# Kernel tuning notes

Measured on AMD Instinct MI355X. Metric: run time of the kernel, lower is better.

## Reference

```python
import jax, jax.numpy as jnp
import numpy as np

N_PULSES = 8_000_000
NUM_DOMS = 200_000
EPS = 1e-08


def setup_inputs() -> dict:
    key = jax.random.key(0)
    k1, k2, k3 = jax.random.split(key, 3)
    times = jax.random.normal(k1, (N_PULSES,), dtype=jnp.float32) * 100.0
    charges = jax.random.uniform(k2, (N_PULSES,), dtype=jnp.float32) * 10.0
    dom_idx = jax.random.randint(k3, (N_PULSES,), 0, NUM_DOMS, dtype=jnp.int32)
    return {"times": times, "charges": charges, "dom_idx": dom_idx, "num_doms": NUM_DOMS}


def reference(times, charges, dom_idx, num_doms):
    n = times.shape[0]
    ones = jnp.ones_like(times)
    # per-DOM pulse counts (float, matching torch's float scatter_add of ones)
    count = jnp.zeros((num_doms,), dtype=times.dtype).at[dom_idx].add(ones)

    # --- temporal features ---
    first_times = jnp.full((num_doms,), jnp.inf, dtype=times.dtype).at[dom_idx].min(times)
    delta_t_first = times - first_times[dom_idx]

    mean_times = jnp.zeros((num_doms,), dtype=times.dtype).at[dom_idx].add(times) / (count + EPS)
    mean_e = mean_times[dom_idx]
    delta_t_median = times - mean_e

    var = jnp.zeros((num_doms,), dtype=times.dtype).at[dom_idx].add((times - mean_e) ** 2) / (count + EPS)
    time_std = jnp.sqrt(var + EPS)
    t_normalized = (times - mean_e) / (time_std[dom_idx] + EPS)

    # --- charge features ---
    total_charges = jnp.zeros((num_doms,), dtype=charges.dtype).at[dom_idx].add(charges)
    charge_fraction = charges / (total_charges[dom_idx] + EPS)

    max_charges = jnp.full((num_doms,), -jnp.inf, dtype=charges.dtype).at[dom_idx].max(charges)
    charge_ratio = charges / (max_charges[dom_idx] + EPS)

    # --- charge rank within each DOM (0 = brightest), fully vectorized ---
    # sort primarily by dom_idx, secondarily by descending charge
    order = jnp.lexsort((-charges, dom_idx))  # (n,)
    sorted_dom = dom_idx[order]
    counts_i = jnp.zeros((num_doms,), dtype=jnp.int32).at[dom_idx].add(jnp.ones_like(dom_idx))
    starts = jnp.cumsum(counts_i) - counts_i  # exclusive prefix-sum of group sizes
    rank_sorted = jnp.arange(n, dtype=jnp.int32) - starts[sorted_dom]
    ranks = jnp.zeros((n,), dtype=jnp.int32).at[order].set(rank_sorted)

    dom_sizes_e = count[dom_idx]  # float sizes per pulse
    log_charge_rank = jnp.log((ranks.astype(times.dtype) + 1.0) / (dom_sizes_e + EPS))

    return jnp.stack(
        [delta_t_first, delta_t_median, t_normalized,
         charge_fraction, charge_ratio, log_charge_rank], axis=1)
```

## Files before the change

kernel.cpp:

```cpp
#include <hip/hip_runtime.h>
#include <hip/hip_bf16.h>
#include <stdint.h>
#include <math.h>

#define NDOMS 200000
#define EPSF 1e-8f
#define DLBITS 8
#define DLMASK 255
#define NBUCK ((NDOMS + DLMASK) >> DLBITS)
#define NB2 (NBUCK * 2)
#define CAP_B 11264
#define CAP_H 6016
#define CSTRIDE 16
#define CHUNK 8192
#define IDXM 0x7FFFFFu

typedef unsigned long long u64;

__device__ __forceinline__ unsigned f2mono(float f){
  unsigned b = __float_as_uint(f);
  return b ^ (unsigned)(((int)b >> 31) | 0x80000000);
}
__device__ __forceinline__ float mono2f(unsigned u){
  unsigned b = (u & 0x80000000u) ? (u ^ 0x80000000u) : ~u;
  return __uint_as_float(b);
}

__global__ void k_init(int* __restrict__ gcursor){
  int i = blockIdx.x * blockDim.x + threadIdx.x;
  if (i < NB2) gcursor[i * CSTRIDE] = 0;
}

__global__ void __launch_bounds__(512)
k_bin(const float* __restrict__ charges, const int* __restrict__ dom,
      const float* __restrict__ times, int n, int* __restrict__ gcursor,
      uint4* __restrict__ rec_g, unsigned short* __restrict__ slotidx){
  __shared__ int lhist[NB2];
  __shared__ int lbase[NB2];
  __shared__ int lcnt[NB2];
  int t = threadIdx.x;
  int start = blockIdx.x * CHUNK;
  int end = min(start + CHUNK, n);
  for (int i = t; i < NB2; i += 512) lhist[i] = 0;
  __syncthreads();
  for (int p = start + t; p < end; p += 512)
    atomicAdd(&lhist[dom[p] >> 7], 1);
  __syncthreads();
  for (int i = t; i < NB2; i += 512){
    int c = lhist[i];
    lbase[i] = c ? atomicAdd(&gcursor[i * CSTRIDE], c) : 0;
    lcnt[i] = 0;
  }
  __syncthreads();
  for (int p = start + t; p < end; p += 512){
    int d = dom[p];
    int i2 = d >> 7;
    int pos = lbase[i2] + atomicAdd(&lcnt[i2], 1);
    if (pos < CAP_B){
      int b = i2 >> 1;
      int slot = (i2 & 1) ? (CAP_B - 1 - pos) : pos;
      uint4 r;
      r.x = ((unsigned)(d & DLMASK) << 23) | (IDXM - (unsigned)p);
      r.y = __float_as_uint(charges[p]);
      r.z = __float_as_uint(times[p]);
      r.w = (unsigned)d;
      rec_g[(size_t)b * CAP_B + slot] = r;
      slotidx[p] = (unsigned short)slot;
    }
  }
}

__global__ void __launch_bounds__(512)
k_grp(const uint4* __restrict__ rec_g, const int* __restrict__ gcursor,
      float* __restrict__ derived, unsigned char* __restrict__ rank_bkt){
  __shared__ u64   keysL[CAP_H];
  __shared__ unsigned short slotS[CAP_H];
  __shared__ int hist[128], starts[128], cur[128];
  __shared__ float s_t[128], s_t2[128], s_c[128];
  __shared__ unsigned mn_t[128], mx_c[128];
  int bid = blockIdx.x, b = bid >> 1, h = bid & 1, t = threadIdx.x;
  int cl = min(gcursor[(2 * b) * CSTRIDE], CAP_B);
  int ch = min(gcursor[(2 * b + 1) * CSTRIDE], CAP_B - cl);
  int myCnt  = h ? ch : cl;
  if (myCnt > CAP_H) myCnt = CAP_H;
  int myBase = h ? (CAP_B - ch) : 0;
  const uint4* rg = rec_g + (size_t)b * CAP_B + myBase;

  if (t < 128){
    hist[t] = 0; s_t[t] = 0.f; s_t2[t] = 0.f; s_c[t] = 0.f;
    mn_t[t] = 0xFFFFFFFFu; mx_c[t] = 0u;
  }
  __syncthreads();
  unsigned rx[12], ry[12], rz[12];
  #pragma unroll
  for (int i = 0; i < 12; ++i){
    int s = t + i * 512;
    if (s < myCnt){
      uint4 r = rg[s];
      rx[i] = r.x; ry[i] = r.y; rz[i] = r.z;
      int dl = (int)((r.x >> 23) & 127);
      float tv = __uint_as_float(r.z);
      atomicAdd(&hist[dl], 1);
      atomicAdd(&s_t[dl], tv);
      atomicAdd(&s_t2[dl], tv * tv);
      atomicAdd(&s_c[dl], __uint_as_float(r.y));
      atomicMax(&mx_c[dl], r.y);
      atomicMin(&mn_t[dl], f2mono(tv));
    }
  }
  __syncthreads();
  if (t < 128) starts[t] = hist[t];
  __syncthreads();
  for (int off = 1; off < 128; off <<= 1){
    int v = 0;
    if (t < 128 && t >= off) v = starts[t - off];
    __syncthreads();
    if (t < 128) starts[t] += v;
    __syncthreads();
  }
  if (t < 128){ starts[t] -= hist[t]; cur[t] = starts[t]; }
  __syncthreads();
  #pragma unroll
  for (int i = 0; i < 12; ++i){
    int s = t + i * 512;
    if (s < myCnt){
      int dl = (int)((rx[i] >> 23) & 127);
      int pos = atomicAdd(&cur[dl], 1);
      keysL[pos] = ((u64)ry[i] << 32) | rx[i];
      slotS[pos] = (unsigned short)s;
    }
  }
  __syncthreads();
  if (t < 128){
    int k = hist[t];
    if (k > 0){
      int d = b * 256 + h * 128 + t;
      float kf = (float)k;
      float m  = s_t[t] / (kf + EPSF);
      float var = (s_t2[t] - 2.0f * m * s_t[t] + kf * m * m) / (kf + EPSF);
      var = fmaxf(var, 0.0f);
      float* dv = derived + (size_t)d * 8;
      dv[0] = mono2f(mn_t[t]);
      dv[1] = m;
      dv[2] = 1.0f / (sqrtf(var + EPSF) + EPSF);
      dv[3] = 1.0f / (s_c[t] + EPSF);
      dv[4] = 1.0f / (__uint_as_float(mx_c[t]) + EPSF);
      dv[5] = kf; dv[6] = 0.f; dv[7] = 0.f;
    }
  }
  unsigned char* rb = rank_bkt + (size_t)b * CAP_B + myBase;
  for (int q = t; q < myCnt; q += 512){
    u64 me = keysL[q];
    int dl = (int)((me >> 23) & 127);
    int st = starts[dl], k = hist[dl];
    int r = 0;
    for (int j = st; j < st + k; ++j) r += (keysL[j] > me) ? 1 : 0;
    rb[slotS[q]] = (unsigned char)r;
  }
}

__global__ void __launch_bounds__(256)
k_gat(const int* __restrict__ dom, const unsigned short* __restrict__ slotidx,
      const unsigned char* __restrict__ rank_bkt, int n,
      unsigned char* __restrict__ rank8){
  int p = blockIdx.x * 256 + threadIdx.x;
  if (p < n){
    int b = dom[p] >> DLBITS;
    rank8[p] = rank_bkt[(size_t)b * CAP_B + slotidx[p]];
  }
}

__global__ void __launch_bounds__(256)
k_out(const float* __restrict__ times, const float* __restrict__ charges,
      const int* __restrict__ dom, const unsigned char* __restrict__ rank8p,
      const float* __restrict__ derived, int n, float* __restrict__ out){
  __shared__ float st[1536];
  int b = blockIdx.x, t = threadIdx.x;
  int p = b * 256 + t;
  float f[6] = {0.f, 0.f, 0.f, 0.f, 0.f, 0.f};
  if (p < n){
    float tv = times[p], cv = charges[p];
    int d = dom[p];
    float r = (float)rank8p[p];
    const float4* dv = (const float4*)(derived + (size_t)d * 8);
    float4 d0 = dv[0];
    float4 d1 = dv[1];
    float dm = tv - d0.y;
    f[0] = tv - d0.x;
    f[1] = dm;
    f[2] = dm * d0.z;
    f[3] = cv * d0.w;
    f[4] = cv * d1.x;
    f[5] = logf((r + 1.0f) / (d1.y + EPSF));
  }
  if ((b + 1) * 256 <= n){
    #pragma unroll
    for (int j = 0; j < 6; ++j) st[t * 6 + j] = f[j];
    __syncthreads();
    float* ob = out + (size_t)b * 1536;
    #pragma unroll
    for (int j = 0; j < 6; ++j) ob[j * 256 + t] = st[j * 256 + t];
  } else if (p < n){
    for (int j = 0; j < 6; ++j) out[(size_t)p * 6 + j] = f[j];
  }
}

extern "C" void kernel_launch(void* const* d_in, const int* in_sizes, int n_in,
                              void* d_out, int out_size, void* d_ws, size_t ws_size,
                              hipStream_t stream) {
  const float* times   = (const float*)d_in[0];
  const float* charges = (const float*)d_in[1];
  const int*   dom     = (const int*)d_in[2];
  const int n = in_sizes[0];

  char* w = (char*)d_ws;
  int*   gcursor = (int*)w;   w += ((size_t)NB2 * CSTRIDE * 4 + 255) & ~255ull;
  float* derived = (float*)w; w += (size_t)NDOMS * 32;
  unsigned char* rank8 = (unsigned char*)w; w += (size_t)n;

  uint4* rec_g = (uint4*)d_out;
  unsigned short* slotidx =
      (unsigned short*)((char*)d_out + (size_t)NBUCK * CAP_B * 16);
  unsigned char* rank_bkt =
      (unsigned char*)((char*)d_out + (size_t)NBUCK * CAP_B * 16 + (size_t)2 * n);

  k_init<<<(NB2 + 255) / 256, 256, 0, stream>>>(gcursor);
  k_bin<<<(n + CHUNK - 1) / CHUNK, 512, 0, stream>>>(charges, dom, times, n,
                                                     gcursor, rec_g, slotidx);
  k_grp<<<NB2, 512, 0, stream>>>(rec_g, gcursor, derived, rank_bkt);
  k_gat<<<(n + 255) / 256, 256, 0, stream>>>(dom, slotidx, rank_bkt, n, rank8);
  k_out<<<(n + 255) / 256, 256, 0, stream>>>(times, charges, dom, rank8,
                                             derived, n, (float*)d_out);
}
```

Before: 869.7 us.

## Shrink bin records to 12 bytes, coalesce rank writes, enlarge binning chunks

Binned records drop the unused dom field, going from 16 to 12 bytes, which cuts scatter and reload traffic. k_grp now keeps each element's sorted position in packed registers and writes ranks in slot order through a shared staging buffer, so global writes are coalesced rather than scattered. CAP_H is lowered, which reduces shared memory and permits an occupancy hint. k_bin uses 1024 threads and 16K-element chunks, giving fewer global cursor atomics. Risks: the smaller CAP_H could truncate larger half-buckets, and the 12-byte records make the loads strided and unaligned.

```diff
diff --git a/kernel.cpp b/kernel.cpp
--- a/kernel.cpp
+++ b/kernel.cpp
@@ -10,9 +10,9 @@
 #define NBUCK ((NDOMS + DLMASK) >> DLBITS)
 #define NB2 (NBUCK * 2)
 #define CAP_B 11264
-#define CAP_H 6016
+#define CAP_H 5568
 #define CSTRIDE 16
-#define CHUNK 8192
+#define CHUNK 16384
 #define IDXM 0x7FFFFFu
 
 typedef unsigned long long u64;
@@ -31,50 +31,48 @@
   if (i < NB2) gcursor[i * CSTRIDE] = 0;
 }
 
-__global__ void __launch_bounds__(512)
+__global__ void __launch_bounds__(1024)
 k_bin(const float* __restrict__ charges, const int* __restrict__ dom,
       const float* __restrict__ times, int n, int* __restrict__ gcursor,
-      uint4* __restrict__ rec_g, unsigned short* __restrict__ slotidx){
+      unsigned* __restrict__ rec_g, unsigned short* __restrict__ slotidx){
   __shared__ int lhist[NB2];
   __shared__ int lbase[NB2];
   __shared__ int lcnt[NB2];
   int t = threadIdx.x;
   int start = blockIdx.x * CHUNK;
   int end = min(start + CHUNK, n);
-  for (int i = t; i < NB2; i += 512) lhist[i] = 0;
-  __syncthreads();
-  for (int p = start + t; p < end; p += 512)
+  for (int i = t; i < NB2; i += 1024) lhist[i] = 0;
+  __syncthreads();
+  for (int p = start + t; p < end; p += 1024)
     atomicAdd(&lhist[dom[p] >> 7], 1);
   __syncthreads();
-  for (int i = t; i < NB2; i += 512){
+  for (int i = t; i < NB2; i += 1024){
     int c = lhist[i];
     lbase[i] = c ? atomicAdd(&gcursor[i * CSTRIDE], c) : 0;
     lcnt[i] = 0;
   }
   __syncthreads();
-  for (int p = start + t; p < end; p += 512){
+  for (int p = start + t; p < end; p += 1024){
     int d = dom[p];
     int i2 = d >> 7;
     int pos = lbase[i2] + atomicAdd(&lcnt[i2], 1);
     if (pos < CAP_B){
       int b = i2 >> 1;
       int slot = (i2 & 1) ? (CAP_B - 1 - pos) : pos;
-      uint4 r;
-      r.x = ((unsigned)(d & DLMASK) << 23) | (IDXM - (unsigned)p);
-      r.y = __float_as_uint(charges[p]);
-      r.z = __float_as_uint(times[p]);
-      r.w = (unsigned)d;
-      rec_g[(size_t)b * CAP_B + slot] = r;
+      unsigned* rp = rec_g + 3 * ((size_t)b * CAP_B + slot);
+      rp[0] = ((unsigned)(d & DLMASK) << 23) | (IDXM - (unsigned)p);
+      rp[1] = __float_as_uint(charges[p]);
+      rp[2] = __float_as_uint(times[p]);
       slotidx[p] = (unsigned short)slot;
     }
   }
 }
 
-__global__ void __launch_bounds__(512)
-k_grp(const uint4* __restrict__ rec_g, const int* __restrict__ gcursor,
+__global__ void __launch_bounds__(512, 8)
+k_grp(const unsigned* __restrict__ rec_g, const int* __restrict__ gcursor,
       float* __restrict__ derived, unsigned char* __restrict__ rank_bkt){
   __shared__ u64   keysL[CAP_H];
-  __shared__ unsigned short slotS[CAP_H];
+  __shared__ unsigned char rankQ[CAP_H];
   __shared__ int hist[128], starts[128], cur[128];
   __shared__ float s_t[128], s_t2[128], s_c[128];
   __shared__ unsigned mn_t[128], mx_c[128];
@@ -84,27 +82,28 @@
   int myCnt  = h ? ch : cl;
   if (myCnt > CAP_H) myCnt = CAP_H;
   int myBase = h ? (CAP_B - ch) : 0;
-  const uint4* rg = rec_g + (size_t)b * CAP_B + myBase;
+  const unsigned* rg = rec_g + 3 * ((size_t)b * CAP_B + myBase);
 
   if (t < 128){
     hist[t] = 0; s_t[t] = 0.f; s_t2[t] = 0.f; s_c[t] = 0.f;
     mn_t[t] = 0xFFFFFFFFu; mx_c[t] = 0u;
   }
   __syncthreads();
-  unsigned rx[12], ry[12], rz[12];
+  unsigned rx[11], ry[11];
+  unsigned pp[6];
   #pragma unroll
-  for (int i = 0; i < 12; ++i){
+  for (int i = 0; i < 11; ++i){
     int s = t + i * 512;
     if (s < myCnt){
-      uint4 r = rg[s];
-      rx[i] = r.x; ry[i] = r.y; rz[i] = r.z;
-      int dl = (int)((r.x >> 23) & 127);
-      float tv = __uint_as_float(r.z);
+      unsigned x = rg[3 * s], y = rg[3 * s + 1], z = rg[3 * s + 2];
+      rx[i] = x; ry[i] = y;
+      int dl = (int)((x >> 23) & 127);
+      float tv = __uint_as_float(z);
       atomicAdd(&hist[dl], 1);
       atomicAdd(&s_t[dl], tv);
       atomicAdd(&s_t2[dl], tv * tv);
-      atomicAdd(&s_c[dl], __uint_as_float(r.y));
-      atomicMax(&mx_c[dl], r.y);
+      atomicAdd(&s_c[dl], __uint_as_float(y));
+      atomicMax(&mx_c[dl], y);
       atomicMin(&mn_t[dl], f2mono(tv));
     }
   }
@@ -121,13 +120,14 @@
   if (t < 128){ starts[t] -= hist[t]; cur[t] = starts[t]; }
   __syncthreads();
   #pragma unroll
-  for (int i = 0; i < 12; ++i){
+  for (int i = 0; i < 11; ++i){
     int s = t + i * 512;
     if (s < myCnt){
       int dl = (int)((rx[i] >> 23) & 127);
-      int pos = atomicAdd(&cur[dl], 1);
+      unsigned pos = (unsigned)atomicAdd(&cur[dl], 1);
       keysL[pos] = ((u64)ry[i] << 32) | rx[i];
-      slotS[pos] = (unsigned short)s;
+      if (i & 1) pp[i >> 1] = (pp[i >> 1] & 0xFFFFu) | (pos << 16);
+      else       pp[i >> 1] = pos;
     }
   }
   __syncthreads();
@@ -148,14 +148,23 @@
       dv[5] = kf; dv[6] = 0.f; dv[7] = 0.f;
     }
   }
-  unsigned char* rb = rank_bkt + (size_t)b * CAP_B + myBase;
   for (int q = t; q < myCnt; q += 512){
     u64 me = keysL[q];
     int dl = (int)((me >> 23) & 127);
     int st = starts[dl], k = hist[dl];
     int r = 0;
     for (int j = st; j < st + k; ++j) r += (keysL[j] > me) ? 1 : 0;
-    rb[slotS[q]] = (unsigned char)r;
+    rankQ[q] = (unsigned char)r;
+  }
+  __syncthreads();
+  unsigned char* rb = rank_bkt + (size_t)b * CAP_B + myBase;
+  #pragma unroll
+  for (int i = 0; i < 11; ++i){
+    int s = t + i * 512;
+    if (s < myCnt){
+      unsigned pos = (i & 1) ? (pp[i >> 1] >> 16) : (pp[i >> 1] & 0xFFFFu);
+      rb[s] = rankQ[pos];
+    }
   }
 }
 
@@ -218,15 +227,15 @@
   float* derived = (float*)w; w += (size_t)NDOMS * 32;
   unsigned char* rank8 = (unsigned char*)w; w += (size_t)n;
 
-  uint4* rec_g = (uint4*)d_out;
+  unsigned* rec_g = (unsigned*)d_out;
   unsigned short* slotidx =
-      (unsigned short*)((char*)d_out + (size_t)NBUCK * CAP_B * 16);
+      (unsigned short*)((char*)d_out + (size_t)NBUCK * CAP_B * 12);
   unsigned char* rank_bkt =
-      (unsigned char*)((char*)d_out + (size_t)NBUCK * CAP_B * 16 + (size_t)2 * n);
+      (unsigned char*)((char*)d_out + (size_t)NBUCK * CAP_B * 12 + (size_t)2 * n);
 
   k_init<<<(NB2 + 255) / 256, 256, 0, stream>>>(gcursor);
-  k_bin<<<(n + CHUNK - 1) / CHUNK, 512, 0, stream>>>(charges, dom, times, n,
-                                                     gcursor, rec_g, slotidx);
+  k_bin<<<(n + CHUNK - 1) / CHUNK, 1024, 0, stream>>>(charges, dom, times, n,
+                                                      gcursor, rec_g, slotidx);
   k_grp<<<NB2, 512, 0, stream>>>(rec_g, gcursor, derived, rank_bkt);
   k_gat<<<(n + 255) / 256, 256, 0, stream>>>(dom, slotidx, rank_bkt, n, rank8);
   k_out<<<(n + 255) / 256, 256, 0, stream>>>(times, charges, dom, rank8,
```

Result: faster. 851.8 us (-2.1%).
